# Optimization experiments

Hardware: AMD Instinct MI355X
Metric: run time of the kernel (lower is better)

## Reference

```python
import jax, jax.numpy as jnp
import numpy as np

NUM_HEADS = 12


def setup_inputs() -> dict:
    key = jax.random.key(0)
    k1, k2, k3 = jax.random.split(key, 3)
    B, N, D = 8, 1024, 768
    x = jax.random.normal(k1, (B, N, D), dtype=jnp.float32)
    Wqkv = jax.random.normal(k2, (D, 3 * D), dtype=jnp.float32) * (D ** -0.5)
    Wproj = jax.random.normal(k3, (D, D), dtype=jnp.float32) * (D ** -0.5)
    bproj = jnp.zeros((D,), dtype=jnp.float32)
    return {"x": x, "Wqkv": Wqkv, "Wproj": Wproj, "bproj": bproj}


def reference(x, Wqkv, Wproj, bproj):
    B, N, D = x.shape
    H = NUM_HEADS
    d = D // H
    scale = d ** -0.5
    qkv = x @ Wqkv  # [B, N, 3D]; qkv_bias=False
    # 'b n (qkv h d) -> qkv b h n d'
    qkv = qkv.reshape(B, N, 3, H, d)
    q = jnp.transpose(qkv[:, :, 0], (0, 2, 1, 3))  # [B, H, N, d]
    k = jnp.transpose(qkv[:, :, 1], (0, 2, 1, 3))
    v = jnp.transpose(qkv[:, :, 2], (0, 2, 1, 3))
    attn = jnp.einsum('bhnd,bhmd->bhnm', q, k) * scale  # [B, H, N, N]
    attn = jax.nn.softmax(attn, axis=-1)
    out = jnp.einsum('bhnm,bhmd->bhnd', attn, v)  # [B, H, N, d]
    out = jnp.transpose(out, (0, 2, 1, 3)).reshape(B, N, D)  # 'b h n d -> b n (h d)'
    return out @ Wproj + bproj
```

## Files before the change

kernel.cpp:

```cpp
#include <hip/hip_runtime.h>
#include <math.h>
#include <stdint.h>

namespace {

constexpr int Nseq = 1024;
constexpr int Dm = 768;
constexpr int threeD = 2304;
constexpr int Mrows = 8192;
constexpr int Hh = 12;
constexpr float kScaleLog2 = 0.18033688011112042f;

using bf16x8 = __attribute__((ext_vector_type(8))) short;
using f32x4 = __attribute__((ext_vector_type(4))) float;
using f32x16 = __attribute__((ext_vector_type(16))) float;
using us4 = __attribute__((ext_vector_type(4))) unsigned short;

__device__ __forceinline__ unsigned short f2bf(float f) {
  union { float f; uint32_t u; } v;
  v.f = f;
  uint32_t r = v.u + 0x7fffu + ((v.u >> 16) & 1u);
  return (unsigned short)(r >> 16);
}

__device__ __forceinline__ float fexp2(float x) {
#if __has_builtin(__builtin_amdgcn_exp2f)
  return __builtin_amdgcn_exp2f(x);
#else
  float r;
  asm("v_exp_f32 %0, %1\n\ts_nop 0" : "=v"(r) : "v"(x));
  return r;
#endif
}

__device__ __forceinline__ uint32_t cvtpk_bf16(float lo, float hi) {
  uint32_t r;
  asm("v_cvt_pk_bf16_f32 %0, %1, %2" : "=v"(r) : "v"(lo), "v"(hi));
  return r;
}

__device__ __forceinline__ void gload_lds16(const void* g, void* l) {
  __builtin_amdgcn_global_load_lds(
      (const __attribute__((address_space(1))) unsigned int*)(uintptr_t)g,
      (__attribute__((address_space(3))) unsigned int*)(uintptr_t)l, 16, 0, 0);
}

__global__ __launch_bounds__(256) void cast_f32_bf16(
    const float* __restrict__ in, unsigned short* __restrict__ outp, int n4) {
  int i = blockIdx.x * blockDim.x + threadIdx.x;
  if (i < n4) {
    float4 v = ((const float4*)in)[i];
    us4 u = {f2bf(v.x), f2bf(v.y), f2bf(v.z), f2bf(v.w)};
    ((us4*)outp)[i] = u;
  }
}

__global__ __launch_bounds__(256) void transpose_cast(
    const float* __restrict__ W, unsigned short* __restrict__ Wt, int K, int N) {
  __shared__ unsigned short tile[32][33];
  const int n0 = blockIdx.x * 32, k0 = blockIdx.y * 32;
  const int tx = threadIdx.x & 31, ty = threadIdx.x >> 5;
#pragma unroll
  for (int i = 0; i < 32; i += 8)
    tile[ty + i][tx] = f2bf(W[(size_t)(k0 + ty + i) * N + n0 + tx]);
  __syncthreads();
#pragma unroll
  for (int i = 0; i < 32; i += 8)
    Wt[(size_t)(n0 + ty + i) * K + k0 + tx] = tile[tx][ty + i];
}

template <int MODE, int BM, int NCOLS>
__global__ __launch_bounds__(256) void gemm_bf16(
    const unsigned short* __restrict__ A, const unsigned short* __restrict__ Bt,
    void* __restrict__ C0, void* __restrict__ C1,
    const float* __restrict__ bias, int K) {
  constexpr int ACH = BM / 16;
  constexpr int TCH = ACH + 8;
  constexpr int MF = BM / 32;
  __shared__ unsigned short As[2][BM * 32];
  __shared__ unsigned short Bs[2][128 * 32];
  const int tid = threadIdx.x;
  const int wid = tid >> 6;
  const int lane = tid & 63;
  const int l15 = lane & 15, lg = lane >> 4;
  const int p = blockIdx.x;
  const int cpx = gridDim.x >> 3;
  const int l = (p & 7) * cpx + (p >> 3);
  const int row0 = (l / NCOLS) * BM, col0 = (l % NCOLS) * 128;
  const int wr = (wid >> 1) * (BM / 2), wc = (wid & 1) * 64;
  const int lr = lane >> 2;
  const int lk = (lane & 3) * 8;

  auto stage = [&](int k0, int bufi) {
#pragma unroll
    for (int it = 0; it < TCH / 4; ++it) {
      const int ci = it * 4 + wid;
      if (ci < ACH) {
        gload_lds16(&A[(size_t)(row0 + ci * 16 + lr) * K + k0 + lk],
                    &As[bufi][ci * 512]);
      } else {
        const int cj = ci - ACH;
        gload_lds16(&Bt[(size_t)(col0 + cj * 16 + lr) * K + k0 + lk],
                    &Bs[bufi][cj * 512]);
      }
    }
  };

  f32x4 acc[MF][4] = {};
  stage(0, 0);
  __syncthreads();
  const int nt = K / 32;
  for (int t = 0; t < nt; ++t) {
    const int cur = t & 1;
    if (t + 1 < nt) stage((t + 1) * 32, cur ^ 1);
    bf16x8 av[MF], bv[4];
#pragma unroll
    for (int m = 0; m < MF; ++m)
      av[m] = *(const bf16x8*)&As[cur][(wr + m * 16 + l15) * 32 + lg * 8];
#pragma unroll
    for (int n = 0; n < 4; ++n)
      bv[n] = *(const bf16x8*)&Bs[cur][(wc + n * 16 + l15) * 32 + lg * 8];
#pragma unroll
    for (int m = 0; m < MF; ++m)
#pragma unroll
      for (int n = 0; n < 4; ++n)
        acc[m][n] =
            __builtin_amdgcn_mfma_f32_16x16x32_bf16(av[m], bv[n], acc[m][n], 0, 0, 0);
    __syncthreads();
  }
  if constexpr (MODE == 1) {
#pragma unroll
    for (int m = 0; m < MF; ++m)
#pragma unroll
      for (int n = 0; n < 4; ++n) {
        const int col = col0 + wc + n * 16 + l15;
#pragma unroll
        for (int rr = 0; rr < 4; ++rr)
          ((float*)C0)[(size_t)(row0 + wr + m * 16 + lg * 4 + rr) * Dm + col] =
              acc[m][n][rr] + bias[col];
      }
  } else if (col0 < 1536) {
#pragma unroll
    for (int m = 0; m < MF; ++m)
#pragma unroll
      for (int n = 0; n < 4; ++n) {
        const int col = col0 + wc + n * 16 + l15;
        const float qs = (col < 768) ? kScaleLog2 : 1.f;
#pragma unroll
        for (int rr = 0; rr < 4; ++rr)
          ((unsigned short*)C0)[(size_t)(row0 + wr + m * 16 + lg * 4 + rr) * 1536 +
                                col] = f2bf(acc[m][n][rr] * qs);
      }
  } else {
#pragma unroll
    for (int m = 0; m < MF; ++m)
#pragma unroll
      for (int n = 0; n < 4; ++n) {
        const int c = col0 + wc + n * 16 + l15 - 1536;
        const int row = row0 + wr + m * 16 + lg * 4;
        const int bb = row >> 10, n0 = row & 1023;
        us4 pk = {f2bf(acc[m][n][0]), f2bf(acc[m][n][1]), f2bf(acc[m][n][2]),
                  f2bf(acc[m][n][3])};
        *(us4*)&((unsigned short*)C1)[((size_t)bb * 768 + c) * 1024 + n0] = pk;
      }
  }
}

__global__ __launch_bounds__(256) void attn_mfma(
    const unsigned short* __restrict__ qkb, const unsigned short* __restrict__ vtb,
    unsigned short* __restrict__ outb) {
  __shared__ unsigned short Ks[2][64 * 64];
  __shared__ unsigned short Vs[2][64 * 64];
  const int tid = threadIdx.x;
  const int wid = tid >> 6, lane = tid & 63;
  const int l31 = lane & 31, hi = lane >> 5;
  const int p = blockIdx.x;
  const int l = (p & 7) * 96 + (p >> 3);
  const int qt = l & 7;
  const int hb = l >> 3;
  const int h = hb % Hh, b = hb / Hh;
  const size_t rb = (size_t)b * Nseq;
  const int hoff = h * 64;
  const size_t vbase = ((size_t)b * 768 + hoff) * 1024;

  const int qrow = qt * 128 + wid * 32 + l31;
  bf16x8 Qf[4];
#pragma unroll
  for (int ks = 0; ks < 4; ++ks)
    Qf[ks] = *(const bf16x8*)&qkb[(rb + qrow) * 1536 + hoff + ks * 16 + hi * 8];

  int strow[2], scol[2];
#pragma unroll
  for (int it = 0; it < 2; ++it) {
    const int ci = it * 256 + wid * 64 + lane;
    const int tr = ci >> 3, cc = ci & 7;
    strow[it] = tr;
    scol[it] = (cc ^ (tr & 7)) * 8;
  }

  auto stage = [&](int kt, int bufi) {
#pragma unroll
    for (int it = 0; it < 2; ++it) {
      const int ldsoff = (it * 256 + wid * 64) * 8;
      gload_lds16(&qkb[(rb + kt * 64 + strow[it]) * 1536 + 768 + hoff + scol[it]],
                  &Ks[bufi][ldsoff]);
      gload_lds16(&vtb[vbase + (size_t)strow[it] * 1024 + kt * 64 + scol[it]],
                  &Vs[bufi][ldsoff]);
    }
  };

  float l_run = 0.f;
  f32x16 o0 = {}, o1 = {};

  stage(0, 0);
  __syncthreads();

  for (int kt = 0; kt < Nseq / 64; ++kt) {
    const int bufi = kt & 1;
    if (kt + 1 < Nseq / 64) stage(kt + 1, bufi ^ 1);
    const unsigned short* ksb = Ks[bufi];
    const unsigned short* vsb = Vs[bufi];
    f32x16 s0 = {}, s1 = {};
    __builtin_amdgcn_s_setprio(1);
#pragma unroll
    for (int ks = 0; ks < 4; ++ks) {
      const int c = 2 * ks + hi;
      {
        const int tr = l31;
        bf16x8 kf = *(const bf16x8*)&ksb[tr * 64 + ((c ^ (tr & 7)) * 8)];
        s0 = __builtin_amdgcn_mfma_f32_32x32x16_bf16(kf, Qf[ks], s0, 0, 0, 0);
      }
      {
        const int tr = l31 + 32;
        bf16x8 kf = *(const bf16x8*)&ksb[tr * 64 + ((c ^ (tr & 7)) * 8)];
        s1 = __builtin_amdgcn_mfma_f32_32x32x16_bf16(kf, Qf[ks], s1, 0, 0, 0);
      }
    }
    __builtin_amdgcn_s_setprio(0);
#pragma unroll
    for (int i = 0; i < 16; ++i) {
      s0[i] = fexp2(s0[i]);
      s1[i] = fexp2(s1[i]);
    }
    float a[8];
#pragma unroll
    for (int i = 0; i < 8; ++i)
      a[i] = (s0[i] + s0[i + 8]) + (s1[i] + s1[i + 8]);
#pragma unroll
    for (int st = 4; st >= 1; st >>= 1)
#pragma unroll
      for (int i = 0; i < st; ++i) a[i] += a[i + st];
    l_run += a[0];
    bf16x8 Pf[4];
#pragma unroll
    for (int ks = 0; ks < 4; ++ks) {
      const f32x16 sv = (ks >> 1) ? s1 : s0;
      const int e0 = 8 * (ks & 1);
      uint32_t pe01 = cvtpk_bf16(sv[e0 + 0], sv[e0 + 1]);
      uint32_t pe23 = cvtpk_bf16(sv[e0 + 2], sv[e0 + 3]);
      uint32_t po01 = cvtpk_bf16(sv[e0 + 4], sv[e0 + 5]);
      uint32_t po23 = cvtpk_bf16(sv[e0 + 6], sv[e0 + 7]);
      asm("v_permlane32_swap_b32 %0, %1" : "+v"(pe01), "+v"(po01));
      asm("v_permlane32_swap_b32 %0, %1" : "+v"(pe23), "+v"(po23));
      union {
        uint32_t w[4];
        bf16x8 v;
      } u;
      u.w[0] = pe01;
      u.w[1] = pe23;
      u.w[2] = po01;
      u.w[3] = po23;
      Pf[ks] = u.v;
    }
    __builtin_amdgcn_s_setprio(1);
#pragma unroll
    for (int ks = 0; ks < 4; ++ks) {
      const int c = 2 * ks + hi;
      {
        const int tr = l31;
        bf16x8 vf = *(const bf16x8*)&vsb[tr * 64 + ((c ^ (tr & 7)) * 8)];
        o0 = __builtin_amdgcn_mfma_f32_32x32x16_bf16(vf, Pf[ks], o0, 0, 0, 0);
      }
      {
        const int tr = l31 + 32;
        bf16x8 vf = *(const bf16x8*)&vsb[tr * 64 + ((c ^ (tr & 7)) * 8)];
        o1 = __builtin_amdgcn_mfma_f32_32x32x16_bf16(vf, Pf[ks], o1, 0, 0, 0);
      }
    }
    __builtin_amdgcn_s_setprio(0);
    __syncthreads();
  }
  const float lsum = l_run + __shfl_xor(l_run, 32);
  const float linv = 1.f / lsum;
  const size_t obase = (size_t)(rb + qrow) * Dm + hoff;
#pragma unroll
  for (int g = 0; g < 4; ++g) {
    us4 a4 = {f2bf(o0[g * 4 + 0] * linv), f2bf(o0[g * 4 + 1] * linv),
              f2bf(o0[g * 4 + 2] * linv), f2bf(o0[g * 4 + 3] * linv)};
    *(us4*)&outb[obase + g * 8 + hi * 4] = a4;
    us4 b4 = {f2bf(o1[g * 4 + 0] * linv), f2bf(o1[g * 4 + 1] * linv),
              f2bf(o1[g * 4 + 2] * linv), f2bf(o1[g * 4 + 3] * linv)};
    *(us4*)&outb[obase + 32 + g * 8 + hi * 4] = b4;
  }
}

}

extern "C" void kernel_launch(void* const* d_in, const int* in_sizes, int n_in,
                              void* d_out, int out_size, void* d_ws,
                              size_t ws_size, hipStream_t stream) {
  (void)in_sizes;
  (void)n_in;
  (void)out_size;
  (void)ws_size;
  const float* x = (const float*)d_in[0];
  const float* Wqkv = (const float*)d_in[1];
  const float* Wproj = (const float*)d_in[2];
  const float* bproj = (const float*)d_in[3];
  float* out = (float*)d_out;

  char* w = (char*)d_ws;
  unsigned short* xb = (unsigned short*)w;
  w += (size_t)Mrows * Dm * 2;
  unsigned short* wqkvt = (unsigned short*)w;
  w += (size_t)threeD * Dm * 2;
  unsigned short* wprojt = (unsigned short*)w;
  w += (size_t)Dm * Dm * 2;
  unsigned short* qkb = (unsigned short*)w;
  w += (size_t)Mrows * 1536 * 2;
  unsigned short* vtb = (unsigned short*)w;
  w += (size_t)96 * 64 * 1024 * 2;
  unsigned short* attnb = (unsigned short*)w;

  cast_f32_bf16<<<(Mrows * Dm / 4 + 255) / 256, 256, 0, stream>>>(
      x, xb, Mrows * Dm / 4);
  transpose_cast<<<dim3(threeD / 32, Dm / 32), 256, 0, stream>>>(
      Wqkv, wqkvt, Dm, threeD);
  transpose_cast<<<dim3(Dm / 32, Dm / 32), 256, 0, stream>>>(Wproj, wprojt, Dm, Dm);
  gemm_bf16<0, 128, 18><<<dim3(1152), 256, 0, stream>>>(
      xb, wqkvt, qkb, vtb, nullptr, Dm);
  attn_mfma<<<dim3(768), 256, 0, stream>>>(qkb, vtb, attnb);
  gemm_bf16<1, 64, 6><<<dim3(768), 256, 0, stream>>>(
      attnb, wprojt, out, nullptr, bproj, Dm);
}
```

Baseline: 123.5 us.

## Triple-buffer GEMM with swizzled LDS and fine-grained vmcnt waits

The GEMM moves from a double-buffered LDS pipeline to a triple-buffered one that prefetches two k-tiles ahead. It uses explicit s_waitcnt vmcnt counts in place of a full __syncthreads, so global-to-LDS loads stay in flight across iterations. The LDS tile layout is changed to an XOR-swizzled row-of-4-chunk layout to reduce bank conflicts on the MFMA operand reads. The attention kernel likewise replaces __syncthreads with partial vmcnt waits plus raw barriers, so the next tile's loads overlap compute. This costs more LDS per block, which may lower occupancy, and depends on hand-counted outstanding-load numbers being correct.

```diff
diff --git a/kernel.cpp b/kernel.cpp
--- a/kernel.cpp
+++ b/kernel.cpp
@@ -74,11 +74,12 @@
     const unsigned short* __restrict__ A, const unsigned short* __restrict__ Bt,
     void* __restrict__ C0, void* __restrict__ C1,
     const float* __restrict__ bias, int K) {
-  constexpr int ACH = BM / 16;
-  constexpr int TCH = ACH + 8;
+  constexpr int ASL = BM * 4;
+  constexpr int TS = ASL + 512;
+  constexpr int LPS = TS / 256;
   constexpr int MF = BM / 32;
-  __shared__ unsigned short As[2][BM * 32];
-  __shared__ unsigned short Bs[2][128 * 32];
+  __shared__ unsigned short As[3][ASL * 8];
+  __shared__ unsigned short Bs[3][512 * 8];
   const int tid = threadIdx.x;
   const int wid = tid >> 6;
   const int lane = tid & 63;
@@ -88,45 +89,63 @@
   const int l = (p & 7) * cpx + (p >> 3);
   const int row0 = (l / NCOLS) * BM, col0 = (l % NCOLS) * 128;
   const int wr = (wid >> 1) * (BM / 2), wc = (wid & 1) * 64;
-  const int lr = lane >> 2;
-  const int lk = (lane & 3) * 8;
 
   auto stage = [&](int k0, int bufi) {
-#pragma unroll
-    for (int it = 0; it < TCH / 4; ++it) {
-      const int ci = it * 4 + wid;
-      if (ci < ACH) {
-        gload_lds16(&A[(size_t)(row0 + ci * 16 + lr) * K + k0 + lk],
-                    &As[bufi][ci * 512]);
+    unsigned short* as = As[bufi];
+    unsigned short* bs = Bs[bufi];
+#pragma unroll
+    for (int it = 0; it < LPS; ++it) {
+      const int s = it * 256 + tid;
+      if (s < ASL) {
+        const int r = s >> 2, c = s & 3;
+        const int g = c ^ ((r >> 1) & 3);
+        gload_lds16(&A[(size_t)(row0 + r) * K + k0 + g * 8],
+                    &as[(s & ~63) * 8]);
       } else {
-        const int cj = ci - ACH;
-        gload_lds16(&Bt[(size_t)(col0 + cj * 16 + lr) * K + k0 + lk],
-                    &Bs[bufi][cj * 512]);
+        const int s2 = s - ASL;
+        const int r = s2 >> 2, c = s2 & 3;
+        const int g = c ^ ((r >> 1) & 3);
+        gload_lds16(&Bt[(size_t)(col0 + r) * K + k0 + g * 8],
+                    &bs[(s2 & ~63) * 8]);
       }
     }
   };
 
   f32x4 acc[MF][4] = {};
+  const int nt = K / 32;
   stage(0, 0);
-  __syncthreads();
-  const int nt = K / 32;
+  stage(32, 1);
   for (int t = 0; t < nt; ++t) {
-    const int cur = t & 1;
-    if (t + 1 < nt) stage((t + 1) * 32, cur ^ 1);
+    const int cur = t % 3;
+    if (t + 2 < nt) {
+      stage((t + 2) * 32, (t + 2) % 3);
+      asm volatile("s_waitcnt vmcnt(%0)" ::"i"(2 * LPS) : "memory");
+    } else if (t + 1 < nt) {
+      asm volatile("s_waitcnt vmcnt(%0)" ::"i"(LPS) : "memory");
+    } else {
+      asm volatile("s_waitcnt vmcnt(0)" ::: "memory");
+    }
+    __builtin_amdgcn_s_barrier();
     bf16x8 av[MF], bv[4];
 #pragma unroll
-    for (int m = 0; m < MF; ++m)
-      av[m] = *(const bf16x8*)&As[cur][(wr + m * 16 + l15) * 32 + lg * 8];
-#pragma unroll
-    for (int n = 0; n < 4; ++n)
-      bv[n] = *(const bf16x8*)&Bs[cur][(wc + n * 16 + l15) * 32 + lg * 8];
+    for (int m = 0; m < MF; ++m) {
+      const int ar = wr + m * 16 + l15;
+      av[m] = *(const bf16x8*)&As[cur][(ar * 4 + (lg ^ ((ar >> 1) & 3))) * 8];
+    }
+#pragma unroll
+    for (int n = 0; n < 4; ++n) {
+      const int br = wc + n * 16 + l15;
+      bv[n] = *(const bf16x8*)&Bs[cur][(br * 4 + (lg ^ ((br >> 1) & 3))) * 8];
+    }
 #pragma unroll
     for (int m = 0; m < MF; ++m)
 #pragma unroll
       for (int n = 0; n < 4; ++n)
         acc[m][n] =
             __builtin_amdgcn_mfma_f32_16x16x32_bf16(av[m], bv[n], acc[m][n], 0, 0, 0);
-    __syncthreads();
+    asm volatile("s_waitcnt lgkmcnt(0)" ::: "memory");
+    __builtin_amdgcn_sched_barrier(0);
+    __builtin_amdgcn_s_barrier();
   }
   if constexpr (MODE == 1) {
 #pragma unroll
@@ -169,6 +188,7 @@
 __global__ __launch_bounds__(256) void attn_mfma(
     const unsigned short* __restrict__ qkb, const unsigned short* __restrict__ vtb,
     unsigned short* __restrict__ outb) {
+  constexpr int NT = Nseq / 64;
   __shared__ unsigned short Ks[2][64 * 64];
   __shared__ unsigned short Vs[2][64 * 64];
   const int tid = threadIdx.x;
@@ -213,11 +233,16 @@
   f32x16 o0 = {}, o1 = {};
 
   stage(0, 0);
-  __syncthreads();
-
-  for (int kt = 0; kt < Nseq / 64; ++kt) {
+
+  for (int kt = 0; kt < NT; ++kt) {
     const int bufi = kt & 1;
-    if (kt + 1 < Nseq / 64) stage(kt + 1, bufi ^ 1);
+    if (kt + 1 < NT) {
+      stage(kt + 1, bufi ^ 1);
+      asm volatile("s_waitcnt vmcnt(4)" ::: "memory");
+    } else {
+      asm volatile("s_waitcnt vmcnt(0)" ::: "memory");
+    }
+    __builtin_amdgcn_s_barrier();
     const unsigned short* ksb = Ks[bufi];
     const unsigned short* vsb = Vs[bufi];
     f32x16 s0 = {}, s1 = {};
@@ -288,7 +313,9 @@
       }
     }
     __builtin_amdgcn_s_setprio(0);
-    __syncthreads();
+    asm volatile("s_waitcnt lgkmcnt(0)" ::: "memory");
+    __builtin_amdgcn_sched_barrier(0);
+    __builtin_amdgcn_s_barrier();
   }
   const float lsum = l_run + __shfl_xor(l_run, 32);
   const float linv = 1.f / lsum;
```

After: 121.3 us. About the same (-1.8%).
